# Kernel optimization log

Hardware: AMD Instinct MI355X
Metric: run time of the kernel (lower is better)

The kernel has to match this reference:

```python
import jax, jax.numpy as jnp
import numpy as np

B, S, D, H = 2, 2048, 1024, 16
HD = D // H  # 64


def setup_inputs() -> dict:
    key = jax.random.key(0)
    k1, k2, k3, k4, k5, k6 = jax.random.split(key, 6)
    x = jax.random.normal(k1, (B, S, D), dtype=jnp.float32)
    # binary mask source (1.0 = masked-out position), multiplied by -1e9 inside
    mask = (jax.random.uniform(k2, (B, S, S), dtype=jnp.float32) < 0.1).astype(jnp.float32)
    lim = 1.0 / np.sqrt(D)
    Wqkv = jax.random.uniform(k3, (D, 3 * D), dtype=jnp.float32, minval=-lim, maxval=lim)
    bqkv = jax.random.uniform(k4, (3 * D,), dtype=jnp.float32, minval=-lim, maxval=lim)
    Wo = jax.random.uniform(k5, (D, D), dtype=jnp.float32, minval=-lim, maxval=lim)
    bo = jax.random.uniform(k6, (D,), dtype=jnp.float32, minval=-lim, maxval=lim)
    return {"x": x, "mask": mask, "Wqkv": Wqkv, "bqkv": bqkv, "Wo": Wo, "bo": bo}


def reference(x, mask, Wqkv, bqkv, Wo, bo):
    b, s, d = x.shape
    qkv = x @ Wqkv + bqkv                              # [B,S,3D]
    qkv = qkv.reshape(b, s, 3, H, HD).transpose(2, 0, 3, 1, 4)  # [3,B,H,S,HD]
    q, k, v = qkv[0], qkv[1], qkv[2]
    scale = 1.0 / jnp.sqrt(jnp.float32(HD))
    scores = jnp.einsum('bhqd,bhkd->bhqk', q, k) * scale
    scores = scores + mask[:, None, :, :] * (-1e9)     # broadcast over heads
    attn = jax.nn.softmax(scores, axis=-1)             # [B,H,S,S]
    values = jnp.einsum('bhqk,bhkd->bhqd', attn, v)    # [B,H,S,HD]
    # faithful to source: permute(1,0,2,3) then reshape(B,S,H*HD)
    values = values.transpose(1, 0, 2, 3).reshape(b, s, H * HD)
    return values @ Wo + bo
```

## Files before the change

### kernel.cpp

```cpp
#include <hip/hip_runtime.h>
#include <stdint.h>

#define BB 2
#define SS 2048
#define DD 1024
#define HH 16
#define HD 64
#define BH 32
#define BS 4096

typedef short bf16x8 __attribute__((ext_vector_type(8)));
typedef float f32x4 __attribute__((ext_vector_type(4)));

static __device__ __forceinline__ unsigned short f2bf(float f) {
    union { float f; unsigned int u; } x;
    x.f = f;
    unsigned int u = x.u;
    unsigned int r = u + 0x7FFFu + ((u >> 16) & 1u);
    return (unsigned short)(r >> 16);
}

static __device__ __forceinline__ void gld16(unsigned short* lds, const unsigned short* g) {
    __builtin_amdgcn_global_load_lds(
        (const __attribute__((address_space(1))) unsigned int*)g,
        (__attribute__((address_space(3))) unsigned int*)lds,
        16, 0, 0);
}

__global__ __launch_bounds__(256) void prep(
    const float* __restrict__ x, unsigned short* __restrict__ xb,
    const float* __restrict__ Wqkv, unsigned short* __restrict__ WqkvT,
    const float* __restrict__ Wo, unsigned short* __restrict__ WoT,
    const float* __restrict__ mask, unsigned int* __restrict__ mbitsT) {
    __shared__ float tile[32][33];
    int bid = blockIdx.x;
    int tid = threadIdx.x;
    if (bid < 4096) {
        int i = (bid * 256 + tid) * 4;
        float4 v = *(const float4*)(x + i);
        ushort4 o;
        o.x = f2bf(v.x); o.y = f2bf(v.y); o.z = f2bf(v.z); o.w = f2bf(v.w);
        *(ushort4*)(xb + i) = o;
    } else if (bid < 8192) {
        const float* W;
        unsigned short* WT;
        int N, t;
        if (bid < 7168) { W = Wqkv; WT = WqkvT; N = 3072; t = bid - 4096; }
        else            { W = Wo;   WT = WoT;   N = 1024; t = bid - 7168; }
        const int K = 1024;
        int nx = N >> 5;
        int n0 = (t % nx) * 32, k0 = (t / nx) * 32;
        int tx = tid & 31, ty = tid >> 5;
#pragma unroll
        for (int i = 0; i < 4; i++)
            tile[ty + i * 8][tx] = W[(size_t)(k0 + ty + i * 8) * N + n0 + tx];
        __syncthreads();
#pragma unroll
        for (int i = 0; i < 4; i++)
            WT[(size_t)(n0 + ty + i * 8) * K + k0 + tx] = f2bf(tile[tx][ty + i * 8]);
    } else {
        size_t i = (size_t)(bid - 8192) * 256 + tid;
        float v = mask[i];
        unsigned long long bal = __ballot(v != 0.0f);
        int lane = tid & 63;
        int kw = (int)((i & 2047) >> 5);
        int sq = (int)((i >> 11) & 2047);
        int b = (int)(i >> 22);
        if (lane == 0)
            mbitsT[((size_t)b * 64 + kw) * 2048 + sq] = (unsigned int)bal;
        else if (lane == 32)
            mbitsT[((size_t)b * 64 + kw) * 2048 + sq] = (unsigned int)(bal >> 32);
    }
}

__global__ __launch_bounds__(256) void qkv_gemm(
    const unsigned short* __restrict__ xb,
    const unsigned short* __restrict__ WqkvT,
    const float* __restrict__ bqkv,
    unsigned short* __restrict__ q_ws,
    unsigned short* __restrict__ k_ws,
    unsigned short* __restrict__ vB) {
    __shared__ unsigned short ldsA[4096], ldsB[4096];
    int gx = blockIdx.x;
    int tid = threadIdx.x;
    int m0 = (gx / 24) * 128, n0 = (gx % 24) * 128;
    int w = tid >> 6, lane = tid & 63, quad = lane >> 4, l15 = lane & 15;

    int r = tid >> 2, p = tid & 3;
    int c = (p - (r >> 1)) & 3;
    const unsigned short* gA0 = xb + (size_t)(m0 + r) * 1024 + c * 8;
    const unsigned short* gA1 = gA0 + (size_t)64 * 1024;
    const unsigned short* gB0 = WqkvT + (size_t)(n0 + r) * 1024 + c * 8;
    const unsigned short* gB1 = gB0 + (size_t)64 * 1024;
    unsigned short* lA0 = ldsA + w * 512;
    unsigned short* lA1 = ldsA + 2048 + w * 512;
    unsigned short* lB0 = ldsB + w * 512;
    unsigned short* lB1 = ldsB + 2048 + w * 512;

    int wm = w >> 1, wn = w & 1;
    int posq = ((quad + (l15 >> 1)) & 3) * 8;
    int aoff = (wm * 64 + l15) * 32 + posq;
    int boff = (wn * 64 + l15) * 32 + posq;

    f32x4 acc[4][4] = {};
    for (int k0 = 0; k0 < 1024; k0 += 32) {
        __syncthreads();
        gld16(lA0, gA0 + k0);
        gld16(lA1, gA1 + k0);
        gld16(lB0, gB0 + k0);
        gld16(lB1, gB1 + k0);
        __syncthreads();
        bf16x8 af[4], bfr[4];
#pragma unroll
        for (int i = 0; i < 4; i++) {
            af[i]  = *(const bf16x8*)(ldsA + aoff + i * 512);
            bfr[i] = *(const bf16x8*)(ldsB + boff + i * 512);
        }
#pragma unroll
        for (int i = 0; i < 4; i++)
#pragma unroll
            for (int j = 0; j < 4; j++)
                acc[i][j] = __builtin_amdgcn_mfma_f32_16x16x32_bf16(af[i], bfr[j], acc[i][j], 0, 0, 0);
    }

    int t = n0 >> 10;
    int ncol0 = n0 + wn * 64;
    int hh = (ncol0 >> 6) & 15;
    int Rb = m0 + wm * 64 + quad * 4;

    if (t == 2) {
        int rowbase = m0 + wm * 64;
        int b = rowbase >> 11;
        int kt = (rowbase >> 6) & 31;
        int bh = b * 16 + hh;
#pragma unroll
        for (int j = 0; j < 4; j++) {
            int hd = j * 16 + l15;
            float bias = bqkv[ncol0 + hd];
#pragma unroll
            for (int i = 0; i < 4; i++) {
                unsigned short* dst = vB +
                    (((((size_t)bh * 32 + kt) * 2 + (i >> 1)) * 4 + quad) * 64 + hd) * 8 + (i & 1) * 4;
                ushort4 pk;
                pk.x = f2bf(acc[i][j][0] + bias);
                pk.y = f2bf(acc[i][j][1] + bias);
                pk.z = f2bf(acc[i][j][2] + bias);
                pk.w = f2bf(acc[i][j][3] + bias);
                *(ushort4*)dst = pk;
            }
        }
    } else {
        unsigned short* dst = (t == 0) ? q_ws : k_ws;
#pragma unroll
        for (int j = 0; j < 4; j++) {
            int hd = j * 16 + l15;
            float bias = bqkv[ncol0 + hd];
#pragma unroll
            for (int i = 0; i < 4; i++) {
                int row = Rb + i * 16;
                int b = row >> 11, s = row & 2047;
                int bh = b * 16 + hh;
#pragma unroll
                for (int rr = 0; rr < 4; rr++)
                    dst[((size_t)(bh * 2048 + s + rr)) * 64 + hd] = f2bf(acc[i][j][rr] + bias);
            }
        }
    }
}

__global__ __launch_bounds__(256) void out_gemm(
    const unsigned short* __restrict__ Amat,
    const unsigned short* __restrict__ WoT,
    const float* __restrict__ bo,
    float* __restrict__ out) {
    __shared__ unsigned short ldsA[4096], ldsB[2048];
    int gx = blockIdx.x;
    int m0 = (gx / 16) * 128, n0 = (gx % 16) * 64;
    int tid = threadIdx.x;
    int w = tid >> 6, lane = tid & 63, quad = lane >> 4, l15 = lane & 15;

    int r = tid >> 2, p = tid & 3;
    int c = (p - (r >> 1)) & 3;
    const unsigned short* gA0 = Amat + (size_t)(m0 + r) * 1024 + c * 8;
    const unsigned short* gA1 = gA0 + (size_t)64 * 1024;
    const unsigned short* gB0 = WoT + (size_t)(n0 + r) * 1024 + c * 8;
    unsigned short* lA0 = ldsA + w * 512;
    unsigned short* lA1 = ldsA + 2048 + w * 512;
    unsigned short* lB0 = ldsB + w * 512;

    int wm = w >> 1, wn = w & 1;
    int posq = ((quad + (l15 >> 1)) & 3) * 8;
    int aoff = (wm * 64 + l15) * 32 + posq;
    int boff = (wn * 32 + l15) * 32 + posq;

    f32x4 acc[4][2] = {};
    for (int k0 = 0; k0 < 1024; k0 += 32) {
        __syncthreads();
        gld16(lA0, gA0 + k0);
        gld16(lA1, gA1 + k0);
        gld16(lB0, gB0 + k0);
        __syncthreads();
        bf16x8 af[4], bfr[2];
#pragma unroll
        for (int i = 0; i < 4; i++) af[i] = *(const bf16x8*)(ldsA + aoff + i * 512);
#pragma unroll
        for (int j = 0; j < 2; j++) bfr[j] = *(const bf16x8*)(ldsB + boff + j * 512);
#pragma unroll
        for (int i = 0; i < 4; i++)
#pragma unroll
            for (int j = 0; j < 2; j++)
                acc[i][j] = __builtin_amdgcn_mfma_f32_16x16x32_bf16(af[i], bfr[j], acc[i][j], 0, 0, 0);
    }
    int ncol0 = n0 + wn * 32;
    int Rb = m0 + wm * 64 + quad * 4;
#pragma unroll
    for (int j = 0; j < 2; j++) {
        int col = ncol0 + j * 16 + l15;
        float bias = bo[col];
#pragma unroll
        for (int i = 0; i < 4; i++) {
            int row = Rb + i * 16;
#pragma unroll
            for (int rr = 0; rr < 4; rr++)
                out[(size_t)(row + rr) * 1024 + col] = acc[i][j][rr] + bias;
        }
    }
}

__global__ __launch_bounds__(256) void attn(
    const unsigned short* __restrict__ q_ws,
    const unsigned short* __restrict__ k_ws,
    const unsigned short* __restrict__ vB,
    const unsigned int* __restrict__ mbitsT,
    unsigned short* __restrict__ o_ws) {
    __shared__ unsigned short ldsK[8192];
    __shared__ unsigned short ldsV[8192];

    int tid = threadIdx.x;
    int w = tid >> 6, lane = tid & 63, quad = lane >> 4, l15 = lane & 15;
    int bxr = blockIdx.x;
    int bx = ((bxr & 7) << 7) | (bxr >> 3);
    int bh = bx >> 5, qt = bx & 31;
    int b = bh >> 4, h = bh & 15;

    int q = qt * 64 + w * 16 + l15;
    const unsigned short* qptr = q_ws + ((size_t)(bh * 2048 + q)) * 64 + quad * 8;
    bf16x8 qf0 = *(const bf16x8*)(qptr);
    bf16x8 qf1 = *(const bf16x8*)(qptr + 32);

    const float c2 = 0.125f * 1.44269504089f;
    const float Cs = c2 * 8388608.0f;
    const float Ds = (127.0f - 16.0f) * 8388608.0f;

    const unsigned int* mb = mbitsT + (size_t)b * 64 * 2048 + q;
    const unsigned short* kbase = k_ws + (size_t)bh * 2048 * 64;
    const unsigned short* vbb = vB + (size_t)bh * 32 * 4096;

    int srow = (lane >> 3);
    int spos = lane & 7;
    unsigned short* dK0 = ldsK + w * 1024 + lane * 8;
    unsigned short* dV0 = ldsV + w * 1024 + lane * 8;
    int r0 = w * 16 + srow;
    int r1 = r0 + 8;
    int g0 = spos ^ (r0 & 7);
    int g1 = spos ^ (r1 & 7);
    const unsigned short* kS0 = kbase + (size_t)r0 * 64 + g0 * 8;
    const unsigned short* kS1 = kbase + (size_t)r1 * 64 + g1 * 8;
    const unsigned short* vS  = vbb + (size_t)w * 1024 + lane * 8;

    f32x4 oacc[4] = {};
    f32x4 lacc = {};
    bf16x8 onesA;
#pragma unroll
    for (int j = 0; j < 8; j++) onesA[j] = (short)0x3F80;

    int sw = (l15 & 7);
    int q4 = quad * 4;

    gld16(dK0, kS0);
    gld16(dK0 + 512, kS1);
    gld16(dV0, vS);
    gld16(dV0 + 512, vS + 512);
    unsigned int mw0 = mb[0];
    unsigned int mw1 = mb[2048];
    __syncthreads();

    for (int kt = 0; kt < 32; kt++) {
        int co = (kt & 1) << 12;

        unsigned int nw0 = 0, nw1 = 0;
        if (kt < 31) {
            int so = co ^ 4096;
            const unsigned short* kn = kS0 + (size_t)(kt + 1) * 4096;
            const unsigned short* kn1 = kS1 + (size_t)(kt + 1) * 4096;
            const unsigned short* vn = vS + (size_t)(kt + 1) * 4096;
            gld16(dK0 + so, kn);
            gld16(dK0 + so + 512, kn1);
            gld16(dV0 + so, vn);
            gld16(dV0 + so + 512, vn + 512);
            nw0 = mb[(size_t)(2 * kt + 2) * 2048];
            nw1 = mb[(size_t)(2 * kt + 3) * 2048];
        }

        const unsigned short* Kc = ldsK + co;
        const unsigned short* Vc = ldsV + co;

        f32x4 sacc[4];
#pragma unroll
        for (int nt = 0; nt < 4; nt++) {
            const unsigned short* kr = Kc + (nt * 16 + l15) * 64;
            bf16x8 kf0, kf1;
            __builtin_memcpy(&kf0, kr + (quad ^ sw) * 8, 16);
            __builtin_memcpy(&kf1, kr + ((quad + 4) ^ sw) * 8, 16);
            f32x4 z = {};
            z = __builtin_amdgcn_mfma_f32_16x16x32_bf16(kf0, qf0, z, 0, 0, 0);
            z = __builtin_amdgcn_mfma_f32_16x16x32_bf16(kf1, qf1, z, 0, 0, 0);
            sacc[nt] = z;
        }
        unsigned int s0 = mw0 >> q4;
        unsigned int s1 = mw1 >> q4;
        unsigned int dw[4][2];
#pragma unroll
        for (int nt = 0; nt < 4; nt++) {
            unsigned int sel = (nt & 2) ? s1 : s0;
            unsigned int u[4];
#pragma unroll
            for (int rr = 0; rr < 4; rr++) {
                float y = __builtin_fmaf(sacc[nt][rr], Cs, Ds);
                if ((sel >> ((nt & 1) * 16 + rr)) & 1u) y = 0.f;
                u[rr] = (unsigned int)(int)y;
            }
            dw[nt][0] = __builtin_amdgcn_perm(u[1], u[0], 0x07060302u);
            dw[nt][1] = __builtin_amdgcn_perm(u[3], u[2], 0x07060302u);
        }
#pragma unroll
        for (int ks2 = 0; ks2 < 2; ks2++) {
            union { bf16x8 v; unsigned int d[4]; } bfr;
            bfr.d[0] = dw[2 * ks2][0];
            bfr.d[1] = dw[2 * ks2][1];
            bfr.d[2] = dw[2 * ks2 + 1][0];
            bfr.d[3] = dw[2 * ks2 + 1][1];
#pragma unroll
            for (int nb = 0; nb < 4; nb++) {
                bf16x8 vf;
                __builtin_memcpy(&vf, Vc + ((ks2 * 4 + quad) * 64 + nb * 16 + l15) * 8, 16);
                oacc[nb] = __builtin_amdgcn_mfma_f32_16x16x32_bf16(vf, bfr.v, oacc[nb], 0, 0, 0);
            }
            lacc = __builtin_amdgcn_mfma_f32_16x16x32_bf16(onesA, bfr.v, lacc, 0, 0, 0);
        }

        __syncthreads();
        mw0 = nw0;
        mw1 = nw1;
    }

    float linv = 1.0f / lacc[0];
    unsigned short* base = o_ws + ((size_t)((h * 2 + b) * 2048 + q)) * 64;
#pragma unroll
    for (int nb = 0; nb < 4; nb++) {
        ushort4 pk;
        pk.x = f2bf(oacc[nb][0] * linv);
        pk.y = f2bf(oacc[nb][1] * linv);
        pk.z = f2bf(oacc[nb][2] * linv);
        pk.w = f2bf(oacc[nb][3] * linv);
        *(ushort4*)(base + nb * 16 + quad * 4) = pk;
    }
}


extern "C" void kernel_launch(void* const* d_in, const int* in_sizes, int n_in,
                              void* d_out, int out_size, void* d_ws, size_t ws_size,
                              hipStream_t stream) {
    const float* x    = (const float*)d_in[0];
    const float* mask = (const float*)d_in[1];
    const float* Wqkv = (const float*)d_in[2];
    const float* bqkv = (const float*)d_in[3];
    const float* Wo   = (const float*)d_in[4];
    const float* bo   = (const float*)d_in[5];
    float* out = (float*)d_out;

    char* ws = (char*)d_ws;
    unsigned short* xb    = (unsigned short*)(ws);
    unsigned short* WqkvT = (unsigned short*)(ws + ((size_t)8 << 20));
    unsigned short* WoT   = (unsigned short*)(ws + ((size_t)14 << 20));
    unsigned short* q_ws  = (unsigned short*)(ws + ((size_t)16 << 20));
    unsigned short* k_ws  = (unsigned short*)(ws + ((size_t)24 << 20));
    unsigned short* vB    = (unsigned short*)(ws + ((size_t)32 << 20));
    unsigned short* o_ws  = (unsigned short*)(ws + ((size_t)40 << 20));
    unsigned int*   mbits = (unsigned int*)(ws + ((size_t)48 << 20));

    prep<<<8192 + 32768, 256, 0, stream>>>(x, xb, Wqkv, WqkvT, Wo, WoT, mask, mbits);
    qkv_gemm<<<768, 256, 0, stream>>>(xb, WqkvT, bqkv, q_ws, k_ws, vB);
    attn<<<1024, 256, 0, stream>>>(q_ws, k_ws, vB, mbits, o_ws);
    out_gemm<<<512, 256, 0, stream>>>(o_ws, WoT, bo, out);
}
```

Baseline: 234.7 us.

## Process two 16-query tiles per wave in attention to reuse K/V LDS loads

Each wave in the attention kernel now handles 32 queries (two 16-row tiles) instead of 16, so every block covers 128 queries and the grid halves from 1024 to 512 blocks. The K and V fragments read from LDS, and the K/V tiles streamed from global memory, are reused across both query tiles. This cuts LDS and global traffic per query. The cost is higher register pressure from the doubled accumulators and fewer blocks, which may lower occupancy and the wave count available to hide latency.

After: 233.6 us. Within noise of the previous version (-0.5%).

```diff
diff --git a/kernel.cpp b/kernel.cpp
--- a/kernel.cpp
+++ b/kernel.cpp
@@ -239,20 +239,24 @@
     int tid = threadIdx.x;
     int w = tid >> 6, lane = tid & 63, quad = lane >> 4, l15 = lane & 15;
     int bxr = blockIdx.x;
-    int bx = ((bxr & 7) << 7) | (bxr >> 3);
-    int bh = bx >> 5, qt = bx & 31;
+    int bx = ((bxr & 7) << 6) | (bxr >> 3);
+    int bh = bx >> 4, qt = bx & 15;
     int b = bh >> 4, h = bh & 15;
 
-    int q = qt * 64 + w * 16 + l15;
-    const unsigned short* qptr = q_ws + ((size_t)(bh * 2048 + q)) * 64 + quad * 8;
-    bf16x8 qf0 = *(const bf16x8*)(qptr);
-    bf16x8 qf1 = *(const bf16x8*)(qptr + 32);
+    int qA = qt * 128 + w * 32 + l15;
+    const unsigned short* qptrA = q_ws + ((size_t)(bh * 2048 + qA)) * 64 + quad * 8;
+    bf16x8 qfA0 = *(const bf16x8*)(qptrA);
+    bf16x8 qfA1 = *(const bf16x8*)(qptrA + 32);
+    const unsigned short* qptrB = qptrA + 16 * 64;
+    bf16x8 qfB0 = *(const bf16x8*)(qptrB);
+    bf16x8 qfB1 = *(const bf16x8*)(qptrB + 32);
 
     const float c2 = 0.125f * 1.44269504089f;
     const float Cs = c2 * 8388608.0f;
     const float Ds = (127.0f - 16.0f) * 8388608.0f;
 
-    const unsigned int* mb = mbitsT + (size_t)b * 64 * 2048 + q;
+    const unsigned int* mbA = mbitsT + (size_t)b * 64 * 2048 + qA;
+    const unsigned int* mbB = mbA + 16;
     const unsigned short* kbase = k_ws + (size_t)bh * 2048 * 64;
     const unsigned short* vbb = vB + (size_t)bh * 32 * 4096;
 
@@ -268,8 +272,8 @@
     const unsigned short* kS1 = kbase + (size_t)r1 * 64 + g1 * 8;
     const unsigned short* vS  = vbb + (size_t)w * 1024 + lane * 8;
 
-    f32x4 oacc[4] = {};
-    f32x4 lacc = {};
+    f32x4 oaccA[4] = {}, oaccB[4] = {};
+    f32x4 laccA = {}, laccB = {};
     bf16x8 onesA;
 #pragma unroll
     for (int j = 0; j < 8; j++) onesA[j] = (short)0x3F80;
@@ -281,14 +285,16 @@
     gld16(dK0 + 512, kS1);
     gld16(dV0, vS);
     gld16(dV0 + 512, vS + 512);
-    unsigned int mw0 = mb[0];
-    unsigned int mw1 = mb[2048];
+    unsigned int mwA0 = mbA[0];
+    unsigned int mwA1 = mbA[2048];
+    unsigned int mwB0 = mbB[0];
+    unsigned int mwB1 = mbB[2048];
     __syncthreads();
 
     for (int kt = 0; kt < 32; kt++) {
         int co = (kt & 1) << 12;
 
-        unsigned int nw0 = 0, nw1 = 0;
+        unsigned int nwA0 = 0, nwA1 = 0, nwB0 = 0, nwB1 = 0;
         if (kt < 31) {
             int so = co ^ 4096;
             const unsigned short* kn = kS0 + (size_t)(kt + 1) * 4096;
@@ -298,72 +304,102 @@
             gld16(dK0 + so + 512, kn1);
             gld16(dV0 + so, vn);
             gld16(dV0 + so + 512, vn + 512);
-            nw0 = mb[(size_t)(2 * kt + 2) * 2048];
-            nw1 = mb[(size_t)(2 * kt + 3) * 2048];
+            nwA0 = mbA[(size_t)(2 * kt + 2) * 2048];
+            nwA1 = mbA[(size_t)(2 * kt + 3) * 2048];
+            nwB0 = mbB[(size_t)(2 * kt + 2) * 2048];
+            nwB1 = mbB[(size_t)(2 * kt + 3) * 2048];
         }
 
         const unsigned short* Kc = ldsK + co;
         const unsigned short* Vc = ldsV + co;
 
-        f32x4 sacc[4];
+        f32x4 saccA[4], saccB[4];
 #pragma unroll
         for (int nt = 0; nt < 4; nt++) {
             const unsigned short* kr = Kc + (nt * 16 + l15) * 64;
             bf16x8 kf0, kf1;
             __builtin_memcpy(&kf0, kr + (quad ^ sw) * 8, 16);
             __builtin_memcpy(&kf1, kr + ((quad + 4) ^ sw) * 8, 16);
-            f32x4 z = {};
-            z = __builtin_amdgcn_mfma_f32_16x16x32_bf16(kf0, qf0, z, 0, 0, 0);
-            z = __builtin_amdgcn_mfma_f32_16x16x32_bf16(kf1, qf1, z, 0, 0, 0);
-            sacc[nt] = z;
-        }
-        unsigned int s0 = mw0 >> q4;
-        unsigned int s1 = mw1 >> q4;
-        unsigned int dw[4][2];
+            f32x4 zA = {};
+            zA = __builtin_amdgcn_mfma_f32_16x16x32_bf16(kf0, qfA0, zA, 0, 0, 0);
+            zA = __builtin_amdgcn_mfma_f32_16x16x32_bf16(kf1, qfA1, zA, 0, 0, 0);
+            saccA[nt] = zA;
+            f32x4 zB = {};
+            zB = __builtin_amdgcn_mfma_f32_16x16x32_bf16(kf0, qfB0, zB, 0, 0, 0);
+            zB = __builtin_amdgcn_mfma_f32_16x16x32_bf16(kf1, qfB1, zB, 0, 0, 0);
+            saccB[nt] = zB;
+        }
+
+        unsigned int sA0 = mwA0 >> q4;
+        unsigned int sA1 = mwA1 >> q4;
+        unsigned int sB0 = mwB0 >> q4;
+        unsigned int sB1 = mwB1 >> q4;
+        unsigned int dwA[4][2], dwB[4][2];
 #pragma unroll
         for (int nt = 0; nt < 4; nt++) {
-            unsigned int sel = (nt & 2) ? s1 : s0;
-            unsigned int u[4];
+            unsigned int selA = (nt & 2) ? sA1 : sA0;
+            unsigned int selB = (nt & 2) ? sB1 : sB0;
+            unsigned int uA[4], uB[4];
 #pragma unroll
             for (int rr = 0; rr < 4; rr++) {
-                float y = __builtin_fmaf(sacc[nt][rr], Cs, Ds);
-                if ((sel >> ((nt & 1) * 16 + rr)) & 1u) y = 0.f;
-                u[rr] = (unsigned int)(int)y;
+                float yA = __builtin_fmaf(saccA[nt][rr], Cs, Ds);
+                if ((selA >> ((nt & 1) * 16 + rr)) & 1u) yA = 0.f;
+                uA[rr] = (unsigned int)(int)yA;
+                float yB = __builtin_fmaf(saccB[nt][rr], Cs, Ds);
+                if ((selB >> ((nt & 1) * 16 + rr)) & 1u) yB = 0.f;
+                uB[rr] = (unsigned int)(int)yB;
             }
-            dw[nt][0] = __builtin_amdgcn_perm(u[1], u[0], 0x07060302u);
-            dw[nt][1] = __builtin_amdgcn_perm(u[3], u[2], 0x07060302u);
-        }
+            dwA[nt][0] = __builtin_amdgcn_perm(uA[1], uA[0], 0x07060302u);
+            dwA[nt][1] = __builtin_amdgcn_perm(uA[3], uA[2], 0x07060302u);
+            dwB[nt][0] = __builtin_amdgcn_perm(uB[1], uB[0], 0x07060302u);
+            dwB[nt][1] = __builtin_amdgcn_perm(uB[3], uB[2], 0x07060302u);
+        }
+
 #pragma unroll
         for (int ks2 = 0; ks2 < 2; ks2++) {
-            union { bf16x8 v; unsigned int d[4]; } bfr;
-            bfr.d[0] = dw[2 * ks2][0];
-            bfr.d[1] = dw[2 * ks2][1];
-            bfr.d[2] = dw[2 * ks2 + 1][0];
-            bfr.d[3] = dw[2 * ks2 + 1][1];
+            union { bf16x8 v; unsigned int d[4]; } bA, bB;
+            bA.d[0] = dwA[2 * ks2][0];
+            bA.d[1] = dwA[2 * ks2][1];
+            bA.d[2] = dwA[2 * ks2 + 1][0];
+            bA.d[3] = dwA[2 * ks2 + 1][1];
+            bB.d[0] = dwB[2 * ks2][0];
+            bB.d[1] = dwB[2 * ks2][1];
+            bB.d[2] = dwB[2 * ks2 + 1][0];
+            bB.d[3] = dwB[2 * ks2 + 1][1];
 #pragma unroll
             for (int nb = 0; nb < 4; nb++) {
                 bf16x8 vf;
                 __builtin_memcpy(&vf, Vc + ((ks2 * 4 + quad) * 64 + nb * 16 + l15) * 8, 16);
-                oacc[nb] = __builtin_amdgcn_mfma_f32_16x16x32_bf16(vf, bfr.v, oacc[nb], 0, 0, 0);
+                oaccA[nb] = __builtin_amdgcn_mfma_f32_16x16x32_bf16(vf, bA.v, oaccA[nb], 0, 0, 0);
+                oaccB[nb] = __builtin_amdgcn_mfma_f32_16x16x32_bf16(vf, bB.v, oaccB[nb], 0, 0, 0);
             }
-            lacc = __builtin_amdgcn_mfma_f32_16x16x32_bf16(onesA, bfr.v, lacc, 0, 0, 0);
-        }
-
-        __syncthreads();
-        mw0 = nw0;
-        mw1 = nw1;
-    }
-
-    float linv = 1.0f / lacc[0];
-    unsigned short* base = o_ws + ((size_t)((h * 2 + b) * 2048 + q)) * 64;
+            laccA = __builtin_amdgcn_mfma_f32_16x16x32_bf16(onesA, bA.v, laccA, 0, 0, 0);
+            laccB = __builtin_amdgcn_mfma_f32_16x16x32_bf16(onesA, bB.v, laccB, 0, 0, 0);
+        }
+
+        __syncthreads();
+        mwA0 = nwA0; mwA1 = nwA1;
+        mwB0 = nwB0; mwB1 = nwB1;
+    }
+
+    float linvA = 1.0f / laccA[0];
+    float linvB = 1.0f / laccB[0];
+    unsigned short* baseA = o_ws + ((size_t)((h * 2 + b) * 2048 + qA)) * 64;
+    unsigned short* baseB = baseA + 16 * 64;
 #pragma unroll
     for (int nb = 0; nb < 4; nb++) {
-        ushort4 pk;
-        pk.x = f2bf(oacc[nb][0] * linv);
-        pk.y = f2bf(oacc[nb][1] * linv);
-        pk.z = f2bf(oacc[nb][2] * linv);
-        pk.w = f2bf(oacc[nb][3] * linv);
-        *(ushort4*)(base + nb * 16 + quad * 4) = pk;
+        ushort4 pkA;
+        pkA.x = f2bf(oaccA[nb][0] * linvA);
+        pkA.y = f2bf(oaccA[nb][1] * linvA);
+        pkA.z = f2bf(oaccA[nb][2] * linvA);
+        pkA.w = f2bf(oaccA[nb][3] * linvA);
+        *(ushort4*)(baseA + nb * 16 + quad * 4) = pkA;
+        ushort4 pkB;
+        pkB.x = f2bf(oaccB[nb][0] * linvB);
+        pkB.y = f2bf(oaccB[nb][1] * linvB);
+        pkB.z = f2bf(oaccB[nb][2] * linvB);
+        pkB.w = f2bf(oaccB[nb][3] * linvB);
+        *(ushort4*)(baseB + nb * 16 + quad * 4) = pkB;
     }
 }
 
@@ -391,6 +427,6 @@
 
     prep<<<8192 + 32768, 256, 0, stream>>>(x, xb, Wqkv, WqkvT, Wo, WoT, mask, mbits);
     qkv_gemm<<<768, 256, 0, stream>>>(xb, WqkvT, bqkv, q_ws, k_ws, vB);
-    attn<<<1024, 256, 0, stream>>>(q_ws, k_ws, vB, mbits, o_ws);
+    attn<<<512, 256, 0, stream>>>(q_ws, k_ws, vB, mbits, o_ws);
     out_gemm<<<512, 256, 0, stream>>>(o_ws, WoT, bo, out);
 }
```
